# Performance work log

Hardware: AMD Instinct MI355X
Metric: run time of the kernel (lower is better)

## Reference

```python
import jax, jax.numpy as jnp
import numpy as np

B, K, D = 512, 16, 256
E = 32            # num_experts
H = int(D * 0.25) # d_hidden = 64


def setup_inputs() -> dict:
    key = jax.random.key(0)
    ks = jax.random.split(key, 7)
    d_rs = D ** -0.5
    h_rs = H ** -0.5
    x = jax.random.normal(ks[0], (B, K, D), dtype=jnp.float32)
    router_w = jax.random.uniform(ks[1], (E, D), jnp.float32, -d_rs, d_rs)
    router_b = jax.random.uniform(ks[2], (E,), jnp.float32, -d_rs, d_rs)
    # init_rsqrt_uniform_(weights1, weights1.shape[-1]) -> bound = H**-0.5
    W1 = jax.random.uniform(ks[3], (E, D, H), jnp.float32, -h_rs, h_rs)
    b1 = jax.random.uniform(ks[4], (E, H), jnp.float32, -h_rs, h_rs)
    # init_rsqrt_uniform_(weights2, weights2.shape[-1]) -> bound = D**-0.5
    W2 = jax.random.uniform(ks[5], (E, H, D), jnp.float32, -d_rs, d_rs)
    b2 = jax.random.uniform(ks[6], (E, D), jnp.float32, -d_rs, d_rs)
    return {"x": x, "router_w": router_w, "router_b": router_b,
            "W1": W1, "b1": b1, "W2": W2, "b2": b2}


def reference(x, router_w, router_b, W1, b1, W2, b2):
    # x: [B, K, D] -> flatten tokens: [N, D]
    xf = x.reshape(-1, D)
    logits = xf @ router_w.T + router_b          # [N, E]
    idx = jnp.argmax(logits, axis=-1)            # [N] top-1 expert per token
    # Gather per-token expert weights (honors top-1 sparsity: N*D*H FLOPs,
    # not E*N*D*H dense dispatch).
    w1t = jnp.take(W1, idx, axis=0)              # [N, D, H]
    h = jnp.einsum('nd,ndh->nh', xf, w1t) + jnp.take(b1, idx, axis=0)
    h = jax.nn.relu(h)                           # act1; dropout p=0 is identity
    w2t = jnp.take(W2, idx, axis=0)              # [N, H, D]
    out = jnp.einsum('nh,nhd->nd', h, w2t) + jnp.take(b2, idx, axis=0)
    out = jax.nn.relu(out)                       # original applies act1 again
    return out.reshape(x.shape)
```

## Files before the change

### kernel.cpp

```cpp
#include <hip/hip_runtime.h>
#include <hip/hip_bf16.h>


constexpr int D = 256;
constexpr int H = 64;
constexpr int E = 32;
constexpr int T_TILE = 16;
constexpr int MAX_TILES = 544;
constexpr int EIDX = 64;
constexpr int PERM = 8256;

__device__ __forceinline__ float quad_reduce(float v) {
    int i1 = __builtin_bit_cast(int, v);
    v += __builtin_bit_cast(float,
        __builtin_amdgcn_mov_dpp(i1, 0xB1, 0xF, 0xF, true));
    int i2 = __builtin_bit_cast(int, v);
    v += __builtin_bit_cast(float,
        __builtin_amdgcn_mov_dpp(i2, 0x4E, 0xF, 0xF, true));
    return v;
}

__global__ __launch_bounds__(256) void router_kernel(
    const float* __restrict__ x, const float* __restrict__ rw,
    const float* __restrict__ rb, int* __restrict__ ws)
{
    __shared__ float4 xs[32][66];
    __shared__ float4 rws[E][66];
    __shared__ float logitS[32][E + 1];
    __shared__ int lcnt[E];

    const int t = threadIdx.x;
    const int n0 = blockIdx.x * 32;
    if (t < E) lcnt[t] = 0;

    const float4* x4 = (const float4*)x;
    const float4* rw4 = (const float4*)rw;
    for (int i = t; i < 32 * 64; i += 256) {
        int r = i >> 6, q = i & 63;
        xs[r][q] = x4[(size_t)(n0 + r) * 64 + q];
        rws[r][q] = rw4[r * 64 + q];
    }
    __syncthreads();

    {
        const int e = t & 31, g = t >> 5;
        float s[4];
#pragma unroll
        for (int j = 0; j < 4; ++j) s[j] = rb[e];
#pragma unroll
        for (int p = 0; p < 8; ++p) {
            float sp[4] = {0.f, 0.f, 0.f, 0.f};
#pragma unroll
            for (int k4 = 0; k4 < 8; ++k4) {
                float4 wv = rws[e][p * 8 + k4];
#pragma unroll
                for (int j = 0; j < 4; ++j) {
                    float4 xv = xs[g * 4 + j][p * 8 + k4];
                    sp[j] = fmaf(xv.x, wv.x, sp[j]);
                    sp[j] = fmaf(xv.y, wv.y, sp[j]);
                    sp[j] = fmaf(xv.z, wv.z, sp[j]);
                    sp[j] = fmaf(xv.w, wv.w, sp[j]);
                }
            }
#pragma unroll
            for (int j = 0; j < 4; ++j) s[j] += sp[j];
        }
#pragma unroll
        for (int j = 0; j < 4; ++j) logitS[g * 4 + j][e] = s[j];
    }
    __syncthreads();

    if (t < 32) {
        float best = logitS[t][0];
        int bi = 0;
#pragma unroll
        for (int i = 1; i < E; ++i) {
            float v = logitS[t][i];
            if (v > best) { best = v; bi = i; }
        }
        ws[EIDX + n0 + t] = bi;
        atomicAdd(&lcnt[bi], 1);
    }
    __syncthreads();
    if (t < E && lcnt[t] > 0) atomicAdd(&ws[t], lcnt[t]);
}

__global__ __launch_bounds__(256) void scatter_kernel(int* __restrict__ ws)
{
    __shared__ int lcnt[E], lbase[E], offs_s[E], cnts[E];
    const int t = threadIdx.x;
    const int n = blockIdx.x * 256 + t;
    if (t < E) { lcnt[t] = 0; cnts[t] = ws[t]; }
    __syncthreads();
    const int e = ws[EIDX + n];
    const int rank = atomicAdd(&lcnt[e], 1);
    __syncthreads();
    if (t < E) {
        int o = 0;
        for (int i = 0; i < E; ++i) if (i < t) o += cnts[i];
        offs_s[t] = o;
        if (lcnt[t] > 0) lbase[t] = atomicAdd(&ws[32 + t], lcnt[t]);
    }
    __syncthreads();
    ws[PERM + offs_s[e] + lbase[e] + rank] = n;
}

__global__ __launch_bounds__(256) void ffn_kernel(
    const float* __restrict__ x,
    const float* __restrict__ W1, const float* __restrict__ b1,
    const float* __restrict__ W2, const float* __restrict__ b2,
    const int* __restrict__ ws, float* __restrict__ out)
{
    __shared__ float part[4][T_TILE][H];
    __shared__ float hsl[T_TILE][H];
    __shared__ int rowsl[T_TILE];
    __shared__ int cs[E];
    __shared__ int info[3];

    const int t = threadIdx.x;
    if (t < E) cs[t] = ws[t];
    __syncthreads();
    if (t == 0) {
        int b = blockIdx.x, off = 0, te = -1, tst = 0, tc = 0;
        for (int e2 = 0; e2 < E; ++e2) {
            const int c = cs[e2];
            const int nt = (c + T_TILE - 1) >> 4;
            if (b < nt) { te = e2; tst = off + b * T_TILE;
                          tc = min(T_TILE, c - b * T_TILE); break; }
            b -= nt; off += c;
        }
        info[0] = te; info[1] = tst; info[2] = tc;
    }
    __syncthreads();
    const int e = info[0];
    if (e < 0) return;
    const int start = info[1];
    const int cnt = info[2];
    const int lane = t & 63;
    const int w = t >> 6;
    const int s = lane & 3;
    const int q = lane >> 2;

    if (t < T_TILE)
        rowsl[t] = ws[PERM + start + (t < cnt ? t : 0)];

    const float* w1e = W1 + (size_t)e * (D * H);
    float w1r[64];
    {
        const float* base = w1e + (w * 4 + s) * 16 * H + q;
#pragma unroll
        for (int j = 0; j < 4; ++j)
#pragma unroll
            for (int k = 0; k < 16; ++k)
                w1r[j * 16 + k] = base[k * H + 16 * j];
    }
    __syncthreads();

#define LOADX(buf, row) {                                                  \
        const float* xb_ = x + (size_t)(row) * D + (w * 4 + s) * 16;       \
        buf[0] = *(const float4*)(xb_ + 0);                                \
        buf[1] = *(const float4*)(xb_ + 4);                                \
        buf[2] = *(const float4*)(xb_ + 8);                                \
        buf[3] = *(const float4*)(xb_ + 12); }

#define BODY1(tok, xb) {                                                   \
        float sp0 = 0.f, sp1 = 0.f, sp2 = 0.f, sp3 = 0.f;                  \
        _Pragma("unroll")                                                  \
        for (int k4 = 0; k4 < 4; ++k4) {                                   \
            float4 xv = xb[k4];                                            \
            _Pragma("unroll")                                              \
            for (int m = 0; m < 4; ++m) {                                  \
                const int k = k4 * 4 + m;                                  \
                const float xs_ = (m == 0) ? xv.x : (m == 1) ? xv.y        \
                                 : (m == 2) ? xv.z : xv.w;                 \
                sp0 = fmaf(xs_, w1r[0 * 16 + k], sp0);                     \
                sp1 = fmaf(xs_, w1r[1 * 16 + k], sp1);                     \
                sp2 = fmaf(xs_, w1r[2 * 16 + k], sp2);                     \
                sp3 = fmaf(xs_, w1r[3 * 16 + k], sp3);                     \
            }                                                              \
        }                                                                  \
        sp0 = quad_reduce(sp0); sp1 = quad_reduce(sp1);                    \
        sp2 = quad_reduce(sp2); sp3 = quad_reduce(sp3);                    \
        float a_ = (s & 1) ? sp1 : sp0;                                    \
        float c_ = (s & 1) ? sp3 : sp2;                                    \
        part[w][tok][q + 16 * s] = (s & 2) ? c_ : a_; }

    {
        float4 xa[4], xb4[4];
        LOADX(xa, rowsl[0]);
        for (int tok = 0; tok < cnt; tok += 2) {
            if (tok + 1 < cnt) LOADX(xb4, rowsl[tok + 1]);
            BODY1(tok, xa);
            if (tok + 1 < cnt) {
                if (tok + 2 < cnt) LOADX(xa, rowsl[tok + 2]);
                BODY1(tok + 1, xb4);
            }
        }
    }

    const float* w2e = W2 + (size_t)e * (H * D);
    float w2r[64];
    {
        const float* base = w2e + 16 * s * D + 64 * w + q;
#pragma unroll
        for (int j = 0; j < 4; ++j)
#pragma unroll
            for (int k = 0; k < 16; ++k)
                w2r[j * 16 + k] = base[k * D + 16 * j];
    }
    const float b2v = b2[e * D + 64 * w + q + 16 * s];
    __syncthreads();

    {
        const int h = t & 63;
        const int tq = t >> 6;
        const float b1v = b1[e * H + h];
#pragma unroll
        for (int r = 0; r < 4; ++r) {
            const int tok = tq * 4 + r;
            if (tok < cnt) {
                float v = part[0][tok][h] + part[1][tok][h]
                        + part[2][tok][h] + part[3][tok][h] + b1v;
                hsl[tok][h] = fmaxf(v, 0.f);
            }
        }
    }
    __syncthreads();

#define LOADH(buf, tok) {                                                  \
        const float* hb_ = &hsl[tok][s * 16];                              \
        buf[0] = *(const float4*)(hb_ + 0);                                \
        buf[1] = *(const float4*)(hb_ + 4);                                \
        buf[2] = *(const float4*)(hb_ + 8);                                \
        buf[3] = *(const float4*)(hb_ + 12); }

#define BODY2(tok, hb) {                                                   \
        float sp0 = 0.f, sp1 = 0.f, sp2 = 0.f, sp3 = 0.f;                  \
        _Pragma("unroll")                                                  \
        for (int k4 = 0; k4 < 4; ++k4) {                                   \
            float4 hv = hb[k4];                                            \
            _Pragma("unroll")                                              \
            for (int m = 0; m < 4; ++m) {                                  \
                const int k = k4 * 4 + m;                                  \
                const float hs_ = (m == 0) ? hv.x : (m == 1) ? hv.y        \
                                 : (m == 2) ? hv.z : hv.w;                 \
                sp0 = fmaf(hs_, w2r[0 * 16 + k], sp0);                     \
                sp1 = fmaf(hs_, w2r[1 * 16 + k], sp1);                     \
                sp2 = fmaf(hs_, w2r[2 * 16 + k], sp2);                     \
                sp3 = fmaf(hs_, w2r[3 * 16 + k], sp3);                     \
            }                                                              \
        }                                                                  \
        sp0 = quad_reduce(sp0); sp1 = quad_reduce(sp1);                    \
        sp2 = quad_reduce(sp2); sp3 = quad_reduce(sp3);                    \
        float a_ = (s & 1) ? sp1 : sp0;                                    \
        float c_ = (s & 1) ? sp3 : sp2;                                    \
        const float val_ = ((s & 2) ? c_ : a_) + b2v;                      \
        const int row_ = rowsl[tok];                                       \
        out[(size_t)row_ * D + 64 * w + q + 16 * s] = fmaxf(val_, 0.f); }

    {
        float4 ha[4], hb4[4];
        LOADH(ha, 0);
        for (int tok = 0; tok < cnt; tok += 2) {
            if (tok + 1 < cnt) LOADH(hb4, tok + 1);
            BODY2(tok, ha);
            if (tok + 1 < cnt) {
                if (tok + 2 < cnt) LOADH(ha, tok + 2);
                BODY2(tok + 1, hb4);
            }
        }
    }
#undef LOADX
#undef BODY1
#undef LOADH
#undef BODY2
}

extern "C" void kernel_launch(void* const* d_in, const int* in_sizes, int n_in,
                              void* d_out, int out_size, void* d_ws, size_t ws_size,
                              hipStream_t stream) {
    const float* x  = (const float*)d_in[0];
    const float* rw = (const float*)d_in[1];
    const float* rb = (const float*)d_in[2];
    const float* W1 = (const float*)d_in[3];
    const float* b1 = (const float*)d_in[4];
    const float* W2 = (const float*)d_in[5];
    const float* b2 = (const float*)d_in[6];
    float* out = (float*)d_out;
    int* ws = (int*)d_ws;

    const int N = in_sizes[0] / D;

    hipMemsetAsync(ws, 0, 256, stream);
    router_kernel<<<N / 32, 256, 0, stream>>>(x, rw, rb, ws);
    scatter_kernel<<<N / 256, 256, 0, stream>>>(ws);
    ffn_kernel<<<MAX_TILES, 256, 0, stream>>>(x, W1, b1, W2, b2, ws, out);
}
```

Baseline: 115.1 us.

## Replace global atomic histogram with per-block counts and drop memset

The router now writes per-block expert histograms to the workspace instead of atomically accumulating global counts. The scatter kernel derives totals and per-block prefix offsets from those histograms, which makes placement deterministic and removes the memset launch and the global atomics. The router weight tile in shared memory is also stored transposed with new padding to change bank-access patterns. In exchange, each scatter block re-reads the full 256x32 histogram.

```diff
diff --git a/kernel.cpp b/kernel.cpp
--- a/kernel.cpp
+++ b/kernel.cpp
@@ -7,8 +7,10 @@
 constexpr int E = 32;
 constexpr int T_TILE = 16;
 constexpr int MAX_TILES = 544;
-constexpr int EIDX = 64;
-constexpr int PERM = 8256;
+constexpr int HIST = 0;
+constexpr int EIDX = 8192;
+constexpr int PERM = 16384;
+constexpr int WCNT = 24576;
 
 __device__ __forceinline__ float quad_reduce(float v) {
     int i1 = __builtin_bit_cast(int, v);
@@ -24,8 +26,8 @@
     const float* __restrict__ x, const float* __restrict__ rw,
     const float* __restrict__ rb, int* __restrict__ ws)
 {
-    __shared__ float4 xs[32][66];
-    __shared__ float4 rws[E][66];
+    __shared__ float4 xs[32][65];
+    __shared__ float4 rwt[64][33];
     __shared__ float logitS[32][E + 1];
     __shared__ int lcnt[E];
 
@@ -38,7 +40,7 @@
     for (int i = t; i < 32 * 64; i += 256) {
         int r = i >> 6, q = i & 63;
         xs[r][q] = x4[(size_t)(n0 + r) * 64 + q];
-        rws[r][q] = rw4[r * 64 + q];
+        rwt[q][r] = rw4[i];
     }
     __syncthreads();
 
@@ -52,7 +54,7 @@
             float sp[4] = {0.f, 0.f, 0.f, 0.f};
 #pragma unroll
             for (int k4 = 0; k4 < 8; ++k4) {
-                float4 wv = rws[e][p * 8 + k4];
+                float4 wv = rwt[p * 8 + k4][e];
 #pragma unroll
                 for (int j = 0; j < 4; ++j) {
                     float4 xv = xs[g * 4 + j][p * 8 + k4];
@@ -82,27 +84,47 @@
         atomicAdd(&lcnt[bi], 1);
     }
     __syncthreads();
-    if (t < E && lcnt[t] > 0) atomicAdd(&ws[t], lcnt[t]);
+    if (t < E) ws[HIST + blockIdx.x * E + t] = lcnt[t];
 }
 
 __global__ __launch_bounds__(256) void scatter_kernel(int* __restrict__ ws)
 {
-    __shared__ int lcnt[E], lbase[E], offs_s[E], cnts[E];
+    __shared__ int cfull[8][E], cbelow[8][E];
+    __shared__ int cnts_s[E], below_s[E], offs_s[E], lcnt[E];
+
     const int t = threadIdx.x;
-    const int n = blockIdx.x * 256 + t;
-    if (t < E) { lcnt[t] = 0; cnts[t] = ws[t]; }
-    __syncthreads();
-    const int e = ws[EIDX + n];
-    const int rank = atomicAdd(&lcnt[e], 1);
+    const int b = blockIdx.x;
+    const int c = t >> 5, e = t & 31;
+    const int rlim = 8 * b;
+
+    int full = 0, below = 0;
+    for (int i = 0; i < 32; ++i) {
+        const int r = c * 32 + i;
+        const int v = ws[HIST + r * E + e];
+        full += v;
+        if (r < rlim) below += v;
+    }
+    cfull[c][e] = full; cbelow[c][e] = below;
     __syncthreads();
     if (t < E) {
-        int o = 0;
-        for (int i = 0; i < E; ++i) if (i < t) o += cnts[i];
-        offs_s[t] = o;
-        if (lcnt[t] > 0) lbase[t] = atomicAdd(&ws[32 + t], lcnt[t]);
-    }
-    __syncthreads();
-    ws[PERM + offs_s[e] + lbase[e] + rank] = n;
+        int tot = 0, bg = 0;
+#pragma unroll
+        for (int c2 = 0; c2 < 8; ++c2) { tot += cfull[c2][t]; bg += cbelow[c2][t]; }
+        cnts_s[t] = tot; below_s[t] = bg; lcnt[t] = 0;
+    }
+    __syncthreads();
+    if (t == 0) {
+        int off = 0;
+        for (int e2 = 0; e2 < E; ++e2) { offs_s[e2] = off; off += cnts_s[e2]; }
+    }
+    __syncthreads();
+    {
+        const int n = b * 256 + t;
+        const int e2 = ws[EIDX + n];
+        const int r = atomicAdd(&lcnt[e2], 1);
+        ws[PERM + offs_s[e2] + below_s[e2] + r] = n;
+    }
+    if (b == 0 && t < E) ws[WCNT + t] = cnts_s[t];
 }
 
 __global__ __launch_bounds__(256) void ffn_kernel(
@@ -118,7 +140,7 @@
     __shared__ int info[3];
 
     const int t = threadIdx.x;
-    if (t < E) cs[t] = ws[t];
+    if (t < E) cs[t] = ws[WCNT + t];
     __syncthreads();
     if (t == 0) {
         int b = blockIdx.x, off = 0, te = -1, tst = 0, tc = 0;
@@ -291,7 +313,6 @@
 
     const int N = in_sizes[0] / D;
 
-    hipMemsetAsync(ws, 0, 256, stream);
     router_kernel<<<N / 32, 256, 0, stream>>>(x, rw, rb, ws);
     scatter_kernel<<<N / 256, 256, 0, stream>>>(ws);
     ffn_kernel<<<MAX_TILES, 256, 0, stream>>>(x, W1, b1, W2, b2, ws, out);
```

Result: faster. 111.2 us (-3.4%).
